# Performance work log

Measured on AMD Instinct MI355X. Metric: run time of the kernel, lower is better.

The kernel has to match this reference:

```python
import jax, jax.numpy as jnp
import numpy as np

V_TH = 1.0  # spikingjelly IFNode default threshold; v starts at 0, hard reset after fire


def setup_inputs() -> dict:
    key = jax.random.key(0)
    k_x, k_w1, k_w2 = jax.random.split(key, 3)
    B, IN, FEAT, OUT = 4096, 3136, 6272, 500
    # binary input spikes (LatencyEncoder emits 0/1 spikes per timestep)
    x = (jax.random.uniform(k_x, (B, IN)) < 0.5).astype(jnp.float32)
    # Linear weights, torch layout [out_features, in_features], kaiming-ish scale
    W1 = jax.random.normal(k_w1, (FEAT, IN), dtype=jnp.float32) / np.sqrt(IN)
    W2 = jax.random.normal(k_w2, (OUT, FEAT), dtype=jnp.float32) / np.sqrt(FEAT)
    return {"x": x, "W1": W1, "W2": W2}


def reference(x, W1, W2):
    # Linear (no bias) -> IF neuron single step: v = 0 + I; spike = (v >= V_TH); hard reset
    v1 = x @ W1.T                      # [B, FEAT]
    s1 = (v1 >= V_TH).astype(x.dtype)  # binary hidden spikes
    v2 = s1 @ W2.T                     # [B, OUT]
    s2 = (v2 >= V_TH).astype(x.dtype)  # output spikes
    return s2
```

## Files before the change

### kernel.cpp

```cpp
#include <hip/hip_runtime.h>


namespace {
constexpr int kB = 4096;
constexpr int kIn = 3136;
constexpr int kFeat = 6272;
constexpr int kFeatWords = 196;
constexpr int kOut = 500;
constexpr size_t kPlane1 = (size_t)kFeat * kIn;
constexpr size_t kW1F = 3 * kPlane1;
constexpr size_t kW2F = (size_t)784 * 12288;
constexpr size_t kS1Bytes = (size_t)kB * kFeatWords * 4;
constexpr size_t kXb2Bytes = (size_t)49 * kB * 8;
constexpr unsigned kCap1 = 2u << 20;
constexpr unsigned kCap2 = 1u << 16;
__device__ constexpr double kTau1 = 7.4769e-4;
__device__ constexpr double kTau2 = 1.4955e-3;
}

typedef int v4i __attribute__((ext_vector_type(4)));
typedef int v16i __attribute__((ext_vector_type(16)));

__device__ __forceinline__ void gload_lds16(const void* g, void* l) {
  __builtin_amdgcn_global_load_lds((__attribute__((address_space(1))) void*)(g),
                                   (__attribute__((address_space(3))) void*)(l),
                                   16, 0, 0);
}

__device__ __forceinline__ v4i expand16(unsigned b) {
  unsigned u0 = (((b      ) & 0xFu) * 0x204081u) & 0x01010101u;
  unsigned u1 = (((b >> 4 ) & 0xFu) * 0x204081u) & 0x01010101u;
  unsigned u2 = (((b >> 8 ) & 0xFu) * 0x204081u) & 0x01010101u;
  unsigned u3 = (((b >> 12) & 0xFu) * 0x204081u) & 0x01010101u;
  return (v4i){(int)u0, (int)u1, (int)u2, (int)u3};
}

__device__ __forceinline__ void split3(float w, signed char* d) {
  float c = rintf(w * 128.f);
  d[0] = (signed char)(int)c;
  float r = fmaf(c, -7.8125e-03f, w);
  c = rintf(r * 16384.f);
  d[1] = (signed char)(int)c;
  r = fmaf(c, -6.103515625e-05f, r);
  c = rintf(r * 2097152.f);
  d[2] = (signed char)(int)c;
}

__global__ __launch_bounds__(256) void conv_w1F(const float* __restrict__ W,
                                                signed char* __restrict__ F) {
  const int bx = blockIdx.x;
  const int fb = bx / 49;
  const int kt = bx % 49;
  const int f = threadIdx.x & 63;
  const int g = threadIdx.x >> 6;
  const float* src = W + (size_t)(fb * 64 + f) * kIn + kt * 64 + g * 16;
  union { signed char c[16]; int4 v; } o[3];
#pragma unroll
  for (int q = 0; q < 4; ++q) {
    const float4 w = *(const float4*)(src + q * 4);
    signed char d[4][3];
    split3(w.x, d[0]); split3(w.y, d[1]); split3(w.z, d[2]); split3(w.w, d[3]);
#pragma unroll
    for (int e = 0; e < 4; ++e)
#pragma unroll
      for (int j = 0; j < 3; ++j) o[j].c[q * 4 + e] = d[e][j];
  }
#pragma unroll
  for (int j = 0; j < 3; ++j)
    *(int4*)(F + ((size_t)bx * 3 + j) * 4096 + g * 1024 + f * 16) = o[j].v;
}

__global__ __launch_bounds__(256) void conv_w2F(const float* __restrict__ W,
                                                signed char* __restrict__ F) {
  const int bx = blockIdx.x;
  const int fb = bx / 98;
  const int kt = bx % 98;
  const int f = threadIdx.x & 63;
  const int g = threadIdx.x >> 6;
  const int feat = fb * 64 + f;
  union { signed char c[16]; int4 v; } o[3];
#pragma unroll
  for (int q = 0; q < 4; ++q) {
    float4 w = {0.f, 0.f, 0.f, 0.f};
    if (feat < kOut)
      w = *(const float4*)(W + (size_t)feat * kFeat + kt * 64 + g * 16 + q * 4);
    signed char d[4][3];
    split3(w.x, d[0]); split3(w.y, d[1]); split3(w.z, d[2]); split3(w.w, d[3]);
#pragma unroll
    for (int e = 0; e < 4; ++e)
#pragma unroll
      for (int j = 0; j < 3; ++j) o[j].c[q * 4 + e] = d[e][j];
  }
#pragma unroll
  for (int j = 0; j < 3; ++j)
    *(int4*)(F + ((size_t)bx * 3 + j) * 4096 + g * 1024 + f * 16) = o[j].v;
}

__global__ __launch_bounds__(256) void pack_x2(const float* __restrict__ X,
                                               uint2* __restrict__ xb2) {
  const int wid = (blockIdx.x * 256 + threadIdx.x) >> 6;
  const int lane = threadIdx.x & 63;
  const int b = wid / 49;
  const int g = wid % 49;
  const float v = X[(size_t)b * kIn + g * 64 + lane];
  const unsigned long long bal = __ballot(v != 0.f);
  if (lane == 0) xb2[(size_t)g * kB + b] = make_uint2((unsigned)bal, (unsigned)(bal >> 32));
}

__global__ __launch_bounds__(256, 2) void fc1_v3(
    const uint2* __restrict__ xb2, const signed char* __restrict__ w1lF,
    unsigned* __restrict__ s1b, unsigned* __restrict__ s1T,
    unsigned* __restrict__ cnt, unsigned* __restrict__ list) {
  __shared__ __align__(16) signed char lds[24576];
  const int tid = threadIdx.x;
  const int lane = tid & 63;
  const int ln31 = lane & 31;
  const int half = lane >> 5;
  const int wv = tid >> 6;
  const int waveM = wv >> 1;
  const int waveN = wv & 1;
  const int bx = blockIdx.x;
  const int bM = blockIdx.y * 256;

  const signed char* const gbase = w1lF + (size_t)bx * 49 * 12288;
  unsigned sG[3], sL[3];
#pragma unroll
  for (int p = 0; p < 3; ++p) {
    const int s = wv + 4 * p;
    sG[p] = s * 1024u + lane * 16u;
    sL[p] = s * 1024u;
  }
  const uint2* const aptr = xb2 + bM + waveM * 128 + ln31;
  const unsigned bfeat = (waveN * 32 + ln31) * 16u;

  v16i acc[4][3] = {};
  uint2 abC[4], abN[4];
#pragma unroll
  for (int m = 0; m < 4; ++m) abC[m] = aptr[m * 32];
#pragma unroll
  for (int p = 0; p < 3; ++p) gload_lds16(gbase + sG[p], lds + sL[p]);

  for (int kt = 0; kt < 49; ++kt) {
    __syncthreads();
    const int cb = (kt & 1) * 12288;
    if (kt < 48) {
      const int nb = ((kt + 1) & 1) * 12288;
      const size_t go = (size_t)(kt + 1) * 12288;
#pragma unroll
      for (int p = 0; p < 3; ++p) gload_lds16(gbase + go + sG[p], lds + nb + sL[p]);
#pragma unroll
      for (int m = 0; m < 4; ++m) abN[m] = aptr[(size_t)(kt + 1) * kB + m * 32];
    }
#pragma unroll
    for (int kk = 0; kk < 2; ++kk) {
      const unsigned gsel = (kk * 2 + half) * 1024u;
      const v4i b0 = *(const v4i*)(lds + cb + 0 * 4096 + gsel + bfeat);
      const v4i b1 = *(const v4i*)(lds + cb + 1 * 4096 + gsel + bfeat);
      const v4i b2 = *(const v4i*)(lds + cb + 2 * 4096 + gsel + bfeat);
#pragma unroll
      for (int m = 0; m < 4; ++m) {
        const unsigned word = kk ? abC[m].y : abC[m].x;
        const v4i a = expand16((word >> (half * 16)) & 0xFFFFu);
        acc[m][0] = __builtin_amdgcn_mfma_i32_32x32x32_i8(a, b0, acc[m][0], 0, 0, 0);
        acc[m][1] = __builtin_amdgcn_mfma_i32_32x32x32_i8(a, b1, acc[m][1], 0, 0, 0);
        acc[m][2] = __builtin_amdgcn_mfma_i32_32x32x32_i8(a, b2, acc[m][2], 0, 0, 0);
      }
    }
#pragma unroll
    for (int m = 0; m < 4; ++m) abC[m] = abN[m];
  }

  const double s7 = 0.0078125;
  const int word = bx * 2 + waveN;
  const int fcol = word * 32 + ln31;
#pragma unroll
  for (int m = 0; m < 4; ++m) {
#pragma unroll
    for (int t = 0; t < 16; ++t) {
      double v = (double)acc[m][2][t];
      v = v * s7 + (double)acc[m][1][t];
      v = v * s7 + (double)acc[m][0][t];
      v = v * s7;
      const unsigned long long bal = __ballot(v >= 1.0);
      const int mrow = bM + waveM * 128 + m * 32 + (t & 3) + 8 * (t >> 2);
      if (lane == 0) {
        s1b[(size_t)mrow * kFeatWords + word] = (unsigned)bal;
        s1T[(size_t)word * kB + mrow] = (unsigned)bal;
      }
      if (lane == 32) {
        s1b[(size_t)(mrow + 4) * kFeatWords + word] = (unsigned)(bal >> 32);
        s1T[(size_t)word * kB + mrow + 4] = (unsigned)(bal >> 32);
      }
      if (fabs(v - 1.0) <= kTau1) {
        const unsigned idx = atomicAdd(cnt, 1u);
        if (idx < kCap1) list[idx] = ((unsigned)(mrow + 4 * half) << 13) | (unsigned)fcol;
      }
    }
  }
}

__global__ __launch_bounds__(256) void fc1_correct(
    const float* __restrict__ x, const float* __restrict__ W1,
    const unsigned* __restrict__ cnt, const unsigned* __restrict__ list,
    unsigned* __restrict__ s1b, unsigned* __restrict__ s1T) {
  const unsigned n = min(cnt[0], kCap1);
  const int lane = threadIdx.x & 63;
  const int wid = (blockIdx.x * 256 + threadIdx.x) >> 6;
  const int nw = (gridDim.x * 256) >> 6;
  for (unsigned i = wid; i < n; i += nw) {
    const unsigned u = list[i];
    const int b = (int)(u >> 13);
    const int f = (int)(u & 8191u);
    double s = 0.0;
    for (int k = lane; k < kIn; k += 64)
      s = fma((double)x[(size_t)b * kIn + k], (double)W1[(size_t)f * kIn + k], s);
#pragma unroll
    for (int off = 32; off > 0; off >>= 1) s += __shfl_down(s, off);
    if (lane == 0) {
      const unsigned mask = 1u << (f & 31);
      unsigned* p1 = s1b + (size_t)b * kFeatWords + (f >> 5);
      unsigned* p2 = s1T + (size_t)(f >> 5) * kB + b;
      if (s >= 1.0) { atomicOr(p1, mask); atomicOr(p2, mask); }
      else          { atomicAnd(p1, ~mask); atomicAnd(p2, ~mask); }
    }
  }
}

__global__ __launch_bounds__(256, 2) void fc2_v3(
    const unsigned* __restrict__ s1T, const signed char* __restrict__ w2lF,
    float* __restrict__ out, unsigned* __restrict__ cnt,
    unsigned* __restrict__ list) {
  __shared__ __align__(16) signed char lds[24576];
  const int tid = threadIdx.x;
  const int lane = tid & 63;
  const int ln31 = lane & 31;
  const int half = lane >> 5;
  const int wv = tid >> 6;
  const int waveM = wv >> 1;
  const int waveN = wv & 1;
  const int bx = blockIdx.x;
  const int bM = blockIdx.y * 128;

  const signed char* const gbase = w2lF + (size_t)bx * 98 * 12288;
  unsigned sG[3], sL[3];
#pragma unroll
  for (int p = 0; p < 3; ++p) {
    const int s = wv + 4 * p;
    sG[p] = s * 1024u + lane * 16u;
    sL[p] = s * 1024u;
  }
  const unsigned* const aptr = s1T + bM + waveM * 64 + ln31;
  const unsigned bfeat = (waveN * 32 + ln31) * 16u;

  v16i acc[2][3] = {};
  unsigned abC[2][2], abN[2][2];
#pragma unroll
  for (int m = 0; m < 2; ++m)
#pragma unroll
    for (int kk = 0; kk < 2; ++kk) abC[m][kk] = aptr[(size_t)kk * kB + m * 32];
#pragma unroll
  for (int p = 0; p < 3; ++p) gload_lds16(gbase + sG[p], lds + sL[p]);

  for (int kt = 0; kt < 98; ++kt) {
    __syncthreads();
    const int cb = (kt & 1) * 12288;
    if (kt < 97) {
      const int nb = ((kt + 1) & 1) * 12288;
      const size_t go = (size_t)(kt + 1) * 12288;
#pragma unroll
      for (int p = 0; p < 3; ++p) gload_lds16(gbase + go + sG[p], lds + nb + sL[p]);
#pragma unroll
      for (int m = 0; m < 2; ++m)
#pragma unroll
        for (int kk = 0; kk < 2; ++kk)
          abN[m][kk] = aptr[((size_t)(kt + 1) * 2 + kk) * kB + m * 32];
    }
#pragma unroll
    for (int kk = 0; kk < 2; ++kk) {
      const unsigned gsel = (kk * 2 + half) * 1024u;
      const v4i b0 = *(const v4i*)(lds + cb + 0 * 4096 + gsel + bfeat);
      const v4i b1 = *(const v4i*)(lds + cb + 1 * 4096 + gsel + bfeat);
      const v4i b2 = *(const v4i*)(lds + cb + 2 * 4096 + gsel + bfeat);
#pragma unroll
      for (int m = 0; m < 2; ++m) {
        const v4i a = expand16((abC[m][kk] >> (half * 16)) & 0xFFFFu);
        acc[m][0] = __builtin_amdgcn_mfma_i32_32x32x32_i8(a, b0, acc[m][0], 0, 0, 0);
        acc[m][1] = __builtin_amdgcn_mfma_i32_32x32x32_i8(a, b1, acc[m][1], 0, 0, 0);
        acc[m][2] = __builtin_amdgcn_mfma_i32_32x32x32_i8(a, b2, acc[m][2], 0, 0, 0);
      }
    }
#pragma unroll
    for (int m = 0; m < 2; ++m) {
      abC[m][0] = abN[m][0];
      abC[m][1] = abN[m][1];
    }
  }

  const double s7 = 0.0078125;
  const int o = bx * 64 + waveN * 32 + ln31;
#pragma unroll
  for (int m = 0; m < 2; ++m) {
#pragma unroll
    for (int t = 0; t < 16; ++t) {
      double v = (double)acc[m][2][t];
      v = v * s7 + (double)acc[m][1][t];
      v = v * s7 + (double)acc[m][0][t];
      v = v * s7;
      const int b = bM + waveM * 64 + m * 32 + (t & 3) + 8 * (t >> 2) + 4 * half;
      if (o < kOut) {
        out[(size_t)b * kOut + o] = (v >= 1.0) ? 1.0f : 0.0f;
        if (fabs(v - 1.0) <= kTau2) {
          const unsigned idx = atomicAdd(cnt, 1u);
          if (idx < kCap2) list[idx] = ((unsigned)b << 13) | (unsigned)o;
        }
      }
    }
  }
}

__global__ __launch_bounds__(256) void fc2_correct(
    const unsigned* __restrict__ s1b, const float* __restrict__ W2,
    const unsigned* __restrict__ cnt, const unsigned* __restrict__ list,
    float* __restrict__ out) {
  const unsigned n = min(cnt[0], kCap2);
  const int lane = threadIdx.x & 63;
  const int wid = (blockIdx.x * 256 + threadIdx.x) >> 6;
  const int nw = (gridDim.x * 256) >> 6;
  for (unsigned i = wid; i < n; i += nw) {
    const unsigned u = list[i];
    const int b = (int)(u >> 13);
    const int o = (int)(u & 8191u);
    double s = 0.0;
    for (int k = lane; k < kFeat; k += 64) {
      const unsigned w = s1b[(size_t)b * kFeatWords + (k >> 5)];
      if ((w >> (k & 31)) & 1u) s += (double)W2[(size_t)o * kFeat + k];
    }
#pragma unroll
    for (int off = 32; off > 0; off >>= 1) s += __shfl_down(s, off);
    if (lane == 0) out[(size_t)b * kOut + o] = (s >= 1.0) ? 1.0f : 0.0f;
  }
}

__global__ __launch_bounds__(256) void snn_fc1(const float* __restrict__ x,
                                               const float* __restrict__ W1,
                                               unsigned int* __restrict__ s1bits) {
  __shared__ double Xd[32][66];
  __shared__ double Wd[32][66];
  __shared__ unsigned int spikes[64][2];
  const int tid = threadIdx.x;
  const int tx = tid & 15;
  const int ty = tid >> 4;
  const int b0 = blockIdx.y * 64;
  const int f0 = blockIdx.x * 64;
  if (tid < 128) spikes[tid >> 1][tid & 1] = 0u;
  double acc[4][4];
#pragma unroll
  for (int j = 0; j < 4; ++j)
#pragma unroll
    for (int i = 0; i < 4; ++i) acc[j][i] = 0.0;
  const int rl = tid >> 2;
  const int kq = (tid & 3) * 8;
  const float* xrow = x + (size_t)(b0 + rl) * kIn + kq;
  const float* wrow = W1 + (size_t)(f0 + rl) * kIn + kq;
  for (int kc = 0; kc < kIn; kc += 32) {
    const float4 xv0 = *(const float4*)(xrow + kc);
    const float4 xv1 = *(const float4*)(xrow + kc + 4);
    const float4 wv0 = *(const float4*)(wrow + kc);
    const float4 wv1 = *(const float4*)(wrow + kc + 4);
    __syncthreads();
    Xd[kq + 0][rl] = (double)xv0.x; Xd[kq + 1][rl] = (double)xv0.y;
    Xd[kq + 2][rl] = (double)xv0.z; Xd[kq + 3][rl] = (double)xv0.w;
    Xd[kq + 4][rl] = (double)xv1.x; Xd[kq + 5][rl] = (double)xv1.y;
    Xd[kq + 6][rl] = (double)xv1.z; Xd[kq + 7][rl] = (double)xv1.w;
    Wd[kq + 0][rl] = (double)wv0.x; Wd[kq + 1][rl] = (double)wv0.y;
    Wd[kq + 2][rl] = (double)wv0.z; Wd[kq + 3][rl] = (double)wv0.w;
    Wd[kq + 4][rl] = (double)wv1.x; Wd[kq + 5][rl] = (double)wv1.y;
    Wd[kq + 6][rl] = (double)wv1.z; Wd[kq + 7][rl] = (double)wv1.w;
    __syncthreads();
#pragma unroll
    for (int k = 0; k < 32; ++k) {
      const double2 xa = *(const double2*)&Xd[k][ty * 4];
      const double2 xb = *(const double2*)&Xd[k][ty * 4 + 2];
      const double2 wa = *(const double2*)&Wd[k][tx * 4];
      const double2 wb = *(const double2*)&Wd[k][tx * 4 + 2];
      const double xv[4] = {xa.x, xa.y, xb.x, xb.y};
      const double wv[4] = {wa.x, wa.y, wb.x, wb.y};
#pragma unroll
      for (int j = 0; j < 4; ++j)
#pragma unroll
        for (int i = 0; i < 4; ++i) acc[j][i] += xv[j] * wv[i];
    }
  }
  __syncthreads();
#pragma unroll
  for (int j = 0; j < 4; ++j) {
    unsigned int nib = 0u;
#pragma unroll
    for (int i = 0; i < 4; ++i) nib |= (acc[j][i] >= 1.0 ? 1u : 0u) << i;
    atomicOr(&spikes[ty * 4 + j][tx >> 3], nib << ((tx * 4) & 31));
  }
  __syncthreads();
  if (tid < 128) {
    const int r = tid >> 1;
    const int w = tid & 1;
    s1bits[(size_t)(b0 + r) * kFeatWords + (f0 >> 5) + w] = spikes[r][w];
  }
}

__global__ __launch_bounds__(256) void snn_fc2(const unsigned int* __restrict__ s1bits,
                                               const float* __restrict__ W2,
                                               float* __restrict__ out) {
  __shared__ double Wd[32][66];
  __shared__ unsigned int Sb[64];
  const int tid = threadIdx.x;
  const int tx = tid & 15;
  const int ty = tid >> 4;
  const int b0 = blockIdx.y * 64;
  const int o0 = blockIdx.x * 64;
  double acc[4][4];
#pragma unroll
  for (int j = 0; j < 4; ++j)
#pragma unroll
    for (int i = 0; i < 4; ++i) acc[j][i] = 0.0;
  const int rl = tid >> 2;
  const int kq = (tid & 3) * 8;
  int orow = o0 + rl;
  if (orow >= kOut) orow = kOut - 1;
  const float* wrow = W2 + (size_t)orow * kFeat + kq;
  for (int kc = 0; kc < kFeat; kc += 32) {
    const float4 wv0 = *(const float4*)(wrow + kc);
    const float4 wv1 = *(const float4*)(wrow + kc + 4);
    unsigned int sword = 0u;
    if (tid < 64) sword = s1bits[(size_t)(b0 + tid) * kFeatWords + (kc >> 5)];
    __syncthreads();
    Wd[kq + 0][rl] = (double)wv0.x; Wd[kq + 1][rl] = (double)wv0.y;
    Wd[kq + 2][rl] = (double)wv0.z; Wd[kq + 3][rl] = (double)wv0.w;
    Wd[kq + 4][rl] = (double)wv1.x; Wd[kq + 5][rl] = (double)wv1.y;
    Wd[kq + 6][rl] = (double)wv1.z; Wd[kq + 7][rl] = (double)wv1.w;
    if (tid < 64) Sb[tid] = sword;
    __syncthreads();
    const unsigned int rw0 = Sb[ty * 4 + 0];
    const unsigned int rw1 = Sb[ty * 4 + 1];
    const unsigned int rw2 = Sb[ty * 4 + 2];
    const unsigned int rw3 = Sb[ty * 4 + 3];
#pragma unroll
    for (int k = 0; k < 32; ++k) {
      const double2 wa = *(const double2*)&Wd[k][tx * 4];
      const double2 wb = *(const double2*)&Wd[k][tx * 4 + 2];
      const double wv[4] = {wa.x, wa.y, wb.x, wb.y};
      const double sv[4] = {(double)((rw0 >> k) & 1u), (double)((rw1 >> k) & 1u),
                            (double)((rw2 >> k) & 1u), (double)((rw3 >> k) & 1u)};
#pragma unroll
      for (int j = 0; j < 4; ++j)
#pragma unroll
        for (int i = 0; i < 4; ++i) acc[j][i] += sv[j] * wv[i];
    }
  }
#pragma unroll
  for (int j = 0; j < 4; ++j) {
    const int b = b0 + ty * 4 + j;
#pragma unroll
    for (int i = 0; i < 4; ++i) {
      const int o = o0 + tx * 4 + i;
      if (o < kOut) out[(size_t)b * kOut + o] = (acc[j][i] >= 1.0) ? 1.0f : 0.0f;
    }
  }
}

extern "C" void kernel_launch(void* const* d_in, const int* in_sizes, int n_in,
                              void* d_out, int out_size, void* d_ws, size_t ws_size,
                              hipStream_t stream) {
  const float* x = (const float*)d_in[0];
  const float* W1 = (const float*)d_in[1];
  const float* W2 = (const float*)d_in[2];
  float* out = (float*)d_out;

  char* p = (char*)d_ws;
  signed char* w1lF = (signed char*)p;   p += kW1F;
  signed char* w2lF = (signed char*)p;   p += kW2F;
  unsigned* s1b = (unsigned*)p;          p += kS1Bytes;
  unsigned* s1T = (unsigned*)p;          p += kS1Bytes;
  uint2* xb2 = (uint2*)p;                p += kXb2Bytes;
  unsigned* list1 = (unsigned*)p;        p += (size_t)kCap1 * 4;
  unsigned* list2 = (unsigned*)p;        p += (size_t)kCap2 * 4;
  unsigned* ctrs = (unsigned*)p;         p += 256;
  const size_t need = (size_t)(p - (char*)d_ws);

  if (ws_size >= need) {
    hipMemsetAsync(ctrs, 0, 32, stream);
    conv_w1F<<<4802, 256, 0, stream>>>(W1, w1lF);
    conv_w2F<<<784, 256, 0, stream>>>(W2, w2lF);
    pack_x2<<<50176, 256, 0, stream>>>(x, xb2);
    fc1_v3<<<dim3(98, 16), 256, 0, stream>>>(xb2, w1lF, s1b, s1T, ctrs, list1);
    fc1_correct<<<1024, 256, 0, stream>>>(x, W1, ctrs, list1, s1b, s1T);
    fc2_v3<<<dim3(8, 32), 256, 0, stream>>>(s1T, w2lF, out, ctrs + 4, list2);
    fc2_correct<<<64, 256, 0, stream>>>(s1b, W2, ctrs + 4, list2, out);
  } else {
    unsigned* s1 = (unsigned*)d_ws;
    snn_fc1<<<dim3(98, 64), 256, 0, stream>>>(x, W1, s1);
    snn_fc2<<<dim3(8, 64), 256, 0, stream>>>(s1, W2, out);
  }
}
```

Before: 613.9 us.

## Use 8-wave blocks in fc1/fc2 and swap grid axes for weight reuse

```diff
diff --git a/kernel.cpp b/kernel.cpp
--- a/kernel.cpp
+++ b/kernel.cpp
@@ -107,7 +107,7 @@
   if (lane == 0) xb2[(size_t)g * kB + b] = make_uint2((unsigned)bal, (unsigned)(bal >> 32));
 }
 
-__global__ __launch_bounds__(256, 2) void fc1_v3(
+__global__ __launch_bounds__(512, 2) void fc1_v4(
     const uint2* __restrict__ xb2, const signed char* __restrict__ w1lF,
     unsigned* __restrict__ s1b, unsigned* __restrict__ s1T,
     unsigned* __restrict__ cnt, unsigned* __restrict__ list) {
@@ -119,26 +119,25 @@
   const int wv = tid >> 6;
   const int waveM = wv >> 1;
   const int waveN = wv & 1;
-  const int bx = blockIdx.x;
-  const int bM = blockIdx.y * 256;
+  const int bx = blockIdx.y;
+  const int bM = blockIdx.x * 256;
 
   const signed char* const gbase = w1lF + (size_t)bx * 49 * 12288;
-  unsigned sG[3], sL[3];
-#pragma unroll
-  for (int p = 0; p < 3; ++p) {
-    const int s = wv + 4 * p;
-    sG[p] = s * 1024u + lane * 16u;
-    sL[p] = s * 1024u;
-  }
-  const uint2* const aptr = xb2 + bM + waveM * 128 + ln31;
+  const bool has1 = (wv < 4);
+  const unsigned sG0 = wv * 1024u + lane * 16u;
+  const unsigned sL0 = wv * 1024u;
+  const unsigned sG1 = (wv + 8) * 1024u + lane * 16u;
+  const unsigned sL1 = (wv + 8) * 1024u;
+
+  const uint2* const aptr = xb2 + bM + waveM * 64 + ln31;
   const unsigned bfeat = (waveN * 32 + ln31) * 16u;
 
-  v16i acc[4][3] = {};
-  uint2 abC[4], abN[4];
-#pragma unroll
-  for (int m = 0; m < 4; ++m) abC[m] = aptr[m * 32];
-#pragma unroll
-  for (int p = 0; p < 3; ++p) gload_lds16(gbase + sG[p], lds + sL[p]);
+  v16i acc[2][3] = {};
+  uint2 abC[2], abN[2];
+#pragma unroll
+  for (int m = 0; m < 2; ++m) abC[m] = aptr[m * 32];
+  gload_lds16(gbase + sG0, lds + sL0);
+  if (has1) gload_lds16(gbase + sG1, lds + sL1);
 
   for (int kt = 0; kt < 49; ++kt) {
     __syncthreads();
@@ -146,10 +145,10 @@
     if (kt < 48) {
       const int nb = ((kt + 1) & 1) * 12288;
       const size_t go = (size_t)(kt + 1) * 12288;
-#pragma unroll
-      for (int p = 0; p < 3; ++p) gload_lds16(gbase + go + sG[p], lds + nb + sL[p]);
-#pragma unroll
-      for (int m = 0; m < 4; ++m) abN[m] = aptr[(size_t)(kt + 1) * kB + m * 32];
+      gload_lds16(gbase + go + sG0, lds + nb + sL0);
+      if (has1) gload_lds16(gbase + go + sG1, lds + nb + sL1);
+#pragma unroll
+      for (int m = 0; m < 2; ++m) abN[m] = aptr[(size_t)(kt + 1) * kB + m * 32];
     }
 #pragma unroll
     for (int kk = 0; kk < 2; ++kk) {
@@ -158,7 +157,7 @@
       const v4i b1 = *(const v4i*)(lds + cb + 1 * 4096 + gsel + bfeat);
       const v4i b2 = *(const v4i*)(lds + cb + 2 * 4096 + gsel + bfeat);
 #pragma unroll
-      for (int m = 0; m < 4; ++m) {
+      for (int m = 0; m < 2; ++m) {
         const unsigned word = kk ? abC[m].y : abC[m].x;
         const v4i a = expand16((word >> (half * 16)) & 0xFFFFu);
         acc[m][0] = __builtin_amdgcn_mfma_i32_32x32x32_i8(a, b0, acc[m][0], 0, 0, 0);
@@ -166,15 +165,15 @@
         acc[m][2] = __builtin_amdgcn_mfma_i32_32x32x32_i8(a, b2, acc[m][2], 0, 0, 0);
       }
     }
-#pragma unroll
-    for (int m = 0; m < 4; ++m) abC[m] = abN[m];
+    abC[0] = abN[0];
+    abC[1] = abN[1];
   }
 
   const double s7 = 0.0078125;
   const int word = bx * 2 + waveN;
   const int fcol = word * 32 + ln31;
 #pragma unroll
-  for (int m = 0; m < 4; ++m) {
+  for (int m = 0; m < 2; ++m) {
 #pragma unroll
     for (int t = 0; t < 16; ++t) {
       double v = (double)acc[m][2][t];
@@ -182,7 +181,7 @@
       v = v * s7 + (double)acc[m][0][t];
       v = v * s7;
       const unsigned long long bal = __ballot(v >= 1.0);
-      const int mrow = bM + waveM * 128 + m * 32 + (t & 3) + 8 * (t >> 2);
+      const int mrow = bM + waveM * 64 + m * 32 + (t & 3) + 8 * (t >> 2);
       if (lane == 0) {
         s1b[(size_t)mrow * kFeatWords + word] = (unsigned)bal;
         s1T[(size_t)word * kB + mrow] = (unsigned)bal;
@@ -226,7 +225,7 @@
   }
 }
 
-__global__ __launch_bounds__(256, 2) void fc2_v3(
+__global__ __launch_bounds__(512, 2) void fc2_v4(
     const unsigned* __restrict__ s1T, const signed char* __restrict__ w2lF,
     float* __restrict__ out, unsigned* __restrict__ cnt,
     unsigned* __restrict__ list) {
@@ -238,28 +237,25 @@
   const int wv = tid >> 6;
   const int waveM = wv >> 1;
   const int waveN = wv & 1;
-  const int bx = blockIdx.x;
-  const int bM = blockIdx.y * 128;
+  const int bx = blockIdx.y;
+  const int bM = blockIdx.x * 128;
 
   const signed char* const gbase = w2lF + (size_t)bx * 98 * 12288;
-  unsigned sG[3], sL[3];
-#pragma unroll
-  for (int p = 0; p < 3; ++p) {
-    const int s = wv + 4 * p;
-    sG[p] = s * 1024u + lane * 16u;
-    sL[p] = s * 1024u;
-  }
-  const unsigned* const aptr = s1T + bM + waveM * 64 + ln31;
+  const bool has1 = (wv < 4);
+  const unsigned sG0 = wv * 1024u + lane * 16u;
+  const unsigned sL0 = wv * 1024u;
+  const unsigned sG1 = (wv + 8) * 1024u + lane * 16u;
+  const unsigned sL1 = (wv + 8) * 1024u;
+
+  const unsigned* const aptr = s1T + bM + waveM * 32 + ln31;
   const unsigned bfeat = (waveN * 32 + ln31) * 16u;
 
-  v16i acc[2][3] = {};
-  unsigned abC[2][2], abN[2][2];
-#pragma unroll
-  for (int m = 0; m < 2; ++m)
-#pragma unroll
-    for (int kk = 0; kk < 2; ++kk) abC[m][kk] = aptr[(size_t)kk * kB + m * 32];
-#pragma unroll
-  for (int p = 0; p < 3; ++p) gload_lds16(gbase + sG[p], lds + sL[p]);
+  v16i acc[3] = {};
+  unsigned abC[2], abN[2];
+#pragma unroll
+  for (int kk = 0; kk < 2; ++kk) abC[kk] = aptr[(size_t)kk * kB];
+  gload_lds16(gbase + sG0, lds + sL0);
+  if (has1) gload_lds16(gbase + sG1, lds + sL1);
 
   for (int kt = 0; kt < 98; ++kt) {
     __syncthreads();
@@ -267,13 +263,11 @@
     if (kt < 97) {
       const int nb = ((kt + 1) & 1) * 12288;
       const size_t go = (size_t)(kt + 1) * 12288;
-#pragma unroll
-      for (int p = 0; p < 3; ++p) gload_lds16(gbase + go + sG[p], lds + nb + sL[p]);
-#pragma unroll
-      for (int m = 0; m < 2; ++m)
-#pragma unroll
-        for (int kk = 0; kk < 2; ++kk)
-          abN[m][kk] = aptr[((size_t)(kt + 1) * 2 + kk) * kB + m * 32];
+      gload_lds16(gbase + go + sG0, lds + nb + sL0);
+      if (has1) gload_lds16(gbase + go + sG1, lds + nb + sL1);
+#pragma unroll
+      for (int kk = 0; kk < 2; ++kk)
+        abN[kk] = aptr[((size_t)(kt + 1) * 2 + kk) * kB];
     }
 #pragma unroll
     for (int kk = 0; kk < 2; ++kk) {
@@ -281,38 +275,29 @@
       const v4i b0 = *(const v4i*)(lds + cb + 0 * 4096 + gsel + bfeat);
       const v4i b1 = *(const v4i*)(lds + cb + 1 * 4096 + gsel + bfeat);
       const v4i b2 = *(const v4i*)(lds + cb + 2 * 4096 + gsel + bfeat);
-#pragma unroll
-      for (int m = 0; m < 2; ++m) {
-        const v4i a = expand16((abC[m][kk] >> (half * 16)) & 0xFFFFu);
-        acc[m][0] = __builtin_amdgcn_mfma_i32_32x32x32_i8(a, b0, acc[m][0], 0, 0, 0);
-        acc[m][1] = __builtin_amdgcn_mfma_i32_32x32x32_i8(a, b1, acc[m][1], 0, 0, 0);
-        acc[m][2] = __builtin_amdgcn_mfma_i32_32x32x32_i8(a, b2, acc[m][2], 0, 0, 0);
-      }
-    }
-#pragma unroll
-    for (int m = 0; m < 2; ++m) {
-      abC[m][0] = abN[m][0];
-      abC[m][1] = abN[m][1];
-    }
+      const v4i a = expand16((abC[kk] >> (half * 16)) & 0xFFFFu);
+      acc[0] = __builtin_amdgcn_mfma_i32_32x32x32_i8(a, b0, acc[0], 0, 0, 0);
+      acc[1] = __builtin_amdgcn_mfma_i32_32x32x32_i8(a, b1, acc[1], 0, 0, 0);
+      acc[2] = __builtin_amdgcn_mfma_i32_32x32x32_i8(a, b2, acc[2], 0, 0, 0);
+    }
+    abC[0] = abN[0];
+    abC[1] = abN[1];
   }
 
   const double s7 = 0.0078125;
   const int o = bx * 64 + waveN * 32 + ln31;
 #pragma unroll
-  for (int m = 0; m < 2; ++m) {
-#pragma unroll
-    for (int t = 0; t < 16; ++t) {
-      double v = (double)acc[m][2][t];
-      v = v * s7 + (double)acc[m][1][t];
-      v = v * s7 + (double)acc[m][0][t];
-      v = v * s7;
-      const int b = bM + waveM * 64 + m * 32 + (t & 3) + 8 * (t >> 2) + 4 * half;
-      if (o < kOut) {
-        out[(size_t)b * kOut + o] = (v >= 1.0) ? 1.0f : 0.0f;
-        if (fabs(v - 1.0) <= kTau2) {
-          const unsigned idx = atomicAdd(cnt, 1u);
-          if (idx < kCap2) list[idx] = ((unsigned)b << 13) | (unsigned)o;
-        }
+  for (int t = 0; t < 16; ++t) {
+    double v = (double)acc[2][t];
+    v = v * s7 + (double)acc[1][t];
+    v = v * s7 + (double)acc[0][t];
+    v = v * s7;
+    const int b = bM + waveM * 32 + (t & 3) + 8 * (t >> 2) + 4 * half;
+    if (o < kOut) {
+      out[(size_t)b * kOut + o] = (v >= 1.0) ? 1.0f : 0.0f;
+      if (fabs(v - 1.0) <= kTau2) {
+        const unsigned idx = atomicAdd(cnt, 1u);
+        if (idx < kCap2) list[idx] = ((unsigned)b << 13) | (unsigned)o;
       }
     }
   }
@@ -491,9 +476,9 @@
     conv_w1F<<<4802, 256, 0, stream>>>(W1, w1lF);
     conv_w2F<<<784, 256, 0, stream>>>(W2, w2lF);
     pack_x2<<<50176, 256, 0, stream>>>(x, xb2);
-    fc1_v3<<<dim3(98, 16), 256, 0, stream>>>(xb2, w1lF, s1b, s1T, ctrs, list1);
+    fc1_v4<<<dim3(16, 98), 512, 0, stream>>>(xb2, w1lF, s1b, s1T, ctrs, list1);
     fc1_correct<<<1024, 256, 0, stream>>>(x, W1, ctrs, list1, s1b, s1T);
-    fc2_v3<<<dim3(8, 32), 256, 0, stream>>>(s1T, w2lF, out, ctrs + 4, list2);
+    fc2_v4<<<dim3(32, 8), 512, 0, stream>>>(s1T, w2lF, out, ctrs + 4, list2);
     fc2_correct<<<64, 256, 0, stream>>>(s1b, W2, ctrs + 4, list2, out);
   } else {
     unsigned* s1 = (unsigned*)d_ws;
```

Measured after the change: 654.5 us. +6.6%, slower.
